# Performance work log

Hardware: AMD Instinct MI355X
Metric: run time of the kernel (lower is better)

Reference implementation:

```python
import jax, jax.numpy as jnp
import numpy as np

B, D, NCOMP, DCOMP = 4096, 2048, 4, 1024  # out_features = NCOMP * DCOMP = 4096


def setup_inputs() -> dict:
    key = jax.random.key(0)
    ks = jax.random.split(key, 6)
    scale = 0.02
    return {
        "x": jax.random.normal(ks[0], (B, D), jnp.float32),
        "noise": jax.random.normal(ks[1], (B, NCOMP), jnp.float32),
        "Wc": jax.random.normal(ks[2], (NCOMP, D, DCOMP), jnp.float32) * scale,
        "bc": jnp.zeros((NCOMP, DCOMP), jnp.float32),
        "Wg": jax.random.normal(ks[3], (D, NCOMP), jnp.float32) * scale,
        "bg": jnp.zeros((NCOMP,), jnp.float32),
        "Wn": jax.random.normal(ks[4], (D, NCOMP), jnp.float32) * scale,
        "bn": jnp.zeros((NCOMP,), jnp.float32),
    }


def reference(x, noise, Wc, bc, Wg, bg, Wn, bn):
    # gating: H = Wg(x) + randn * softplus(Wnoise(x))
    g = x @ Wg + bg                                   # [B, n]
    sp = jax.nn.softplus(x @ Wn + bn)                 # [B, n]
    H = g + noise * sp                                # [B, n]
    # top-1 index, monotonic hard gate: select all components i <= argmax
    k = jnp.argmax(H, axis=1, keepdims=True)          # [B, 1]
    mask = (jnp.arange(H.shape[1])[None, :] <= k).astype(H.dtype)  # [B, n]
    # straight-through: forward value = mask, grad d G/d H = identity
    G = H + jax.lax.stop_gradient(mask - H)
    # all components computed vectorized; unselected ones are zeroed by G
    comps = jnp.einsum('bd,ndo->bno', x, Wc) + bc     # [B, n, DCOMP]
    mask_sg = jax.lax.stop_gradient(mask)
    # multiply by mask_sg so unselected (padded) channels carry no grad path,
    # matching torch which never computes components beyond k (zero pad).
    E = (comps * G[:, :, None] * mask_sg[:, :, None]).reshape(x.shape[0], -1)  # [B, out_features]
    return (E, G)
```

## Files before the change

kernel.cpp:

```cpp
#include <hip/hip_runtime.h>
#include <hip/hip_bf16.h>
#include <math.h>

constexpr int BROWS = 4096;
constexpr int DDIM  = 2048;
constexpr int NCOMP = 4;
constexpr int DCOMP = 1024;
constexpr int NOUT  = NCOMP * DCOMP;

typedef __attribute__((ext_vector_type(8))) short bf16x8;
typedef __attribute__((ext_vector_type(4))) float f32x4;
typedef __attribute__((ext_vector_type(4))) short s16x4;

__device__ __forceinline__ short f2bf(float f) {
  union { float f; unsigned u; } v; v.f = f;
  unsigned r = v.u + 0x7FFFu + ((v.u >> 16) & 1u);
  return (short)(r >> 16);
}

#define GLOAD_LDS16(gptr, lptr) __builtin_amdgcn_global_load_lds( \
    (const __attribute__((address_space(1))) void*)(gptr),        \
    (__attribute__((address_space(3))) void*)(lptr), 16, 0, 0)

__global__ __launch_bounds__(256) void prep_kernel(
    const float* __restrict__ x, const float* __restrict__ noise,
    const float* __restrict__ Wg, const float* __restrict__ bg,
    const float* __restrict__ Wn, const float* __restrict__ bn,
    const float* __restrict__ Wc,
    float* __restrict__ Gout, short* __restrict__ xb, short* __restrict__ WcT) {
  __shared__ float tile[64][65];
  const int bid = blockIdx.x;
  const int tid = threadIdx.x;

  if (bid < 1024) {
    const int lane = tid & 63;
    const int row  = bid * 4 + (tid >> 6);
    const float* xr = x + (size_t)row * DDIM;
    short* xbr = xb + (size_t)row * DDIM;

    float ag[4] = {0.f, 0.f, 0.f, 0.f};
    float an[4] = {0.f, 0.f, 0.f, 0.f};
#pragma unroll
    for (int i = 0; i < 8; i++) {
      int d = i * 256 + lane * 4;
      float4 v = *reinterpret_cast<const float4*>(xr + d);
      s16x4 s; s.x = f2bf(v.x); s.y = f2bf(v.y); s.z = f2bf(v.z); s.w = f2bf(v.w);
      *reinterpret_cast<s16x4*>(xbr + d) = s;
      float xv[4] = {v.x, v.y, v.z, v.w};
#pragma unroll
      for (int j = 0; j < 4; j++) {
        float4 wg = *reinterpret_cast<const float4*>(Wg + 4 * (d + j));
        float4 wn = *reinterpret_cast<const float4*>(Wn + 4 * (d + j));
        ag[0] += xv[j] * wg.x; ag[1] += xv[j] * wg.y;
        ag[2] += xv[j] * wg.z; ag[3] += xv[j] * wg.w;
        an[0] += xv[j] * wn.x; an[1] += xv[j] * wn.y;
        an[2] += xv[j] * wn.z; an[3] += xv[j] * wn.w;
      }
    }
#pragma unroll
    for (int off = 32; off > 0; off >>= 1) {
#pragma unroll
      for (int c = 0; c < 4; c++) {
        ag[c] += __shfl_xor(ag[c], off);
        an[c] += __shfl_xor(an[c], off);
      }
    }
    if (lane == 0) {
      float H[4];
#pragma unroll
      for (int c = 0; c < 4; c++) {
        float v  = an[c] + bn[c];
        float sp = (v > 20.f) ? v : log1pf(expf(v));
        H[c] = (ag[c] + bg[c]) + noise[(size_t)row * NCOMP + c] * sp;
      }
      int k = 0; float best = H[0];
#pragma unroll
      for (int c = 1; c < 4; c++) { if (H[c] > best) { best = H[c]; k = c; } }
#pragma unroll
      for (int c = 0; c < 4; c++)
        Gout[(size_t)row * NCOMP + c] = (c <= k) ? 1.0f : 0.0f;
    }
  } else {
    const int tb  = bid - 1024;
    const int o_t = tb & 15, d_t = (tb >> 4) & 31, c = tb >> 9;
    const int d0 = d_t * 64, o0 = o_t * 64;
    const int col = tid & 63, rb = tid >> 6;

    const float* src = Wc + ((size_t)c * DDIM + d0) * DCOMP + o0;
#pragma unroll
    for (int i = 0; i < 16; i++) {
      int r = rb + i * 4;
      tile[r][col] = src[(size_t)r * DCOMP + col];
    }
    __syncthreads();
    short* dst = WcT + ((size_t)c * DCOMP + o0) * DDIM + d0;
    const int o   = tid >> 2;
    const int dsb = (tid & 3) * 16;
    bf16x8 p0, p1;
#pragma unroll
    for (int k = 0; k < 8; k++) {
      p0[k] = f2bf(tile[dsb + k][o]);
      p1[k] = f2bf(tile[dsb + 8 + k][o]);
    }
    *reinterpret_cast<bf16x8*>(dst + (size_t)o * DDIM + dsb)     = p0;
    *reinterpret_cast<bf16x8*>(dst + (size_t)o * DDIM + dsb + 8) = p1;
  }
}

constexpr int BM = 256, BN = 256, BK = 64;
constexpr int NT = DDIM / BK;
constexpr int HS = 128 * 64;

template<int MB, int NB>
__device__ __forceinline__ void MF(f32x4 (&acc)[8][4], bf16x8 (&a)[4][2], bf16x8 (&b)[2][2]) {
#pragma unroll
  for (int kh = 0; kh < 2; kh++)
#pragma unroll
    for (int ml = 0; ml < 4; ml++)
#pragma unroll
      for (int nl = 0; nl < 2; nl++)
        acc[MB + ml][NB + nl] = __builtin_amdgcn_mfma_f32_16x16x32_bf16(
            a[ml][kh], b[nl][kh], acc[MB + ml][NB + nl], 0, 0, 0);
}

#define PH_SYNC_MFMA(MB, NB, BREG)                           \
  __builtin_amdgcn_sched_barrier(0);                         \
  __builtin_amdgcn_s_barrier();                              \
  asm volatile("s_waitcnt lgkmcnt(0)");                      \
  __builtin_amdgcn_s_setprio(1);                             \
  MF<MB, NB>(acc, a, BREG);                                  \
  __builtin_amdgcn_s_setprio(0);

__global__ __launch_bounds__(512, 2) void gemm_kernel(
    const short* __restrict__ xb, const short* __restrict__ wt,
    const float* __restrict__ bc, const float* __restrict__ G,
    float* __restrict__ E) {
  __shared__ short Asm[2][2][HS];
  __shared__ short Bsm[2][2][HS];

  const int tid  = threadIdx.x;
  const int wave = tid >> 6, lane = tid & 63;
  const int wm = wave >> 2, wn = wave & 3;
  const int fr = lane & 15, fq = lane >> 4, l7 = lane & 7;

  const int xcd = blockIdx.x & 7, j = blockIdx.x >> 3;
  const int trow0 = (((xcd >> 1) << 2) + (j & 3)) * BM;
  const int tcol0 = (((xcd & 1) << 3) + (j >> 2)) * BN;

  const short* baseA[2] = { xb + (size_t)(trow0      ) * DDIM,
                            xb + (size_t)(trow0 + 128) * DDIM };
  const short* baseB[2] = { wt + (size_t)(tcol0      ) * DDIM,
                            wt + (size_t)(tcol0 + 128) * DDIM };

  size_t soff[2]; int ldst[2];
#pragma unroll
  for (int l = 0; l < 2; l++) {
    int f = l * 512 + tid;
    int r = f >> 3;
    int s = (f & 7) ^ (r & 7);
    soff[l] = (size_t)r * DDIM + s * 8;
    ldst[l] = (l * 512 + wave * 64) * 8;
  }

  auto STAGE = [&](const short* gb, int t, short* ldsh) {
#pragma unroll
    for (int l = 0; l < 2; l++)
      GLOAD_LDS16(gb + t * 64 + soff[l], ldsh + ldst[l]);
  };
  auto LDA = [&](const short* Ah, bf16x8 (&a)[4][2]) {
#pragma unroll
    for (int ml = 0; ml < 4; ml++) {
      int rh = wm * 64 + ml * 16 + fr;
#pragma unroll
      for (int kh = 0; kh < 2; kh++) {
        int sl = ((kh * 4 + fq) ^ l7) * 8;
        a[ml][kh] = *reinterpret_cast<const bf16x8*>(Ah + rh * 64 + sl);
      }
    }
  };
  auto LDB = [&](const short* Bh, bf16x8 (&b)[2][2]) {
#pragma unroll
    for (int nl = 0; nl < 2; nl++) {
      int ch = wn * 32 + nl * 16 + fr;
#pragma unroll
      for (int kh = 0; kh < 2; kh++) {
        int sl = ((kh * 4 + fq) ^ l7) * 8;
        b[nl][kh] = *reinterpret_cast<const bf16x8*>(Bh + ch * 64 + sl);
      }
    }
  };

  f32x4 acc[8][4];
#pragma unroll
  for (int m = 0; m < 8; m++)
#pragma unroll
    for (int n = 0; n < 4; n++) acc[m][n] = f32x4{0.f, 0.f, 0.f, 0.f};
  bf16x8 a[4][2], bA[2][2], bB[2][2];

  STAGE(baseA[0], 0, &Asm[0][0][0]);
  STAGE(baseB[0], 0, &Bsm[0][0][0]);
  STAGE(baseB[1], 0, &Bsm[0][1][0]);
  STAGE(baseA[1], 0, &Asm[0][1][0]);
  STAGE(baseA[0], 1, &Asm[1][0][0]);
  STAGE(baseB[0], 1, &Bsm[1][0][0]);
  STAGE(baseB[1], 1, &Bsm[1][1][0]);
  asm volatile("s_waitcnt vmcnt(6)" ::: "memory");
  __builtin_amdgcn_s_barrier();

  for (int i = 0; i < NT / 2 - 1; i++) {
    const int t1 = 2 * i + 1, t2 = 2 * i + 2, t3 = 2 * i + 3;

    LDA(&Asm[0][0][0], a); LDB(&Bsm[0][0][0], bA);
    STAGE(baseA[1], t1, &Asm[1][1][0]);
    PH_SYNC_MFMA(0, 0, bA);
    __builtin_amdgcn_s_barrier();
    LDB(&Bsm[0][1][0], bB);
    STAGE(baseA[0], t2, &Asm[0][0][0]);
    PH_SYNC_MFMA(0, 2, bB);
    __builtin_amdgcn_s_barrier();
    LDA(&Asm[0][1][0], a);
    STAGE(baseB[0], t2, &Bsm[0][0][0]);
    PH_SYNC_MFMA(4, 2, bB);
    __builtin_amdgcn_s_barrier();
    STAGE(baseB[1], t2, &Bsm[0][1][0]);
    PH_SYNC_MFMA(4, 0, bA);
    asm volatile("s_waitcnt vmcnt(6)" ::: "memory");
    __builtin_amdgcn_s_barrier();
    LDA(&Asm[1][0][0], a); LDB(&Bsm[1][0][0], bA);
    STAGE(baseA[1], t2, &Asm[0][1][0]);
    PH_SYNC_MFMA(0, 0, bA);
    __builtin_amdgcn_s_barrier();
    LDB(&Bsm[1][1][0], bB);
    STAGE(baseA[0], t3, &Asm[1][0][0]);
    PH_SYNC_MFMA(0, 2, bB);
    __builtin_amdgcn_s_barrier();
    LDA(&Asm[1][1][0], a);
    STAGE(baseB[0], t3, &Bsm[1][0][0]);
    PH_SYNC_MFMA(4, 2, bB);
    __builtin_amdgcn_s_barrier();
    STAGE(baseB[1], t3, &Bsm[1][1][0]);
    PH_SYNC_MFMA(4, 0, bA);
    asm volatile("s_waitcnt vmcnt(6)" ::: "memory");
    __builtin_amdgcn_s_barrier();
  }

  {
    LDA(&Asm[0][0][0], a); LDB(&Bsm[0][0][0], bA);
    STAGE(baseA[1], NT - 1, &Asm[1][1][0]);
    PH_SYNC_MFMA(0, 0, bA);
    __builtin_amdgcn_s_barrier();
    LDB(&Bsm[0][1][0], bB);
    PH_SYNC_MFMA(0, 2, bB);
    __builtin_amdgcn_s_barrier();
    LDA(&Asm[0][1][0], a);
    PH_SYNC_MFMA(4, 2, bB);
    __builtin_amdgcn_s_barrier();
    PH_SYNC_MFMA(4, 0, bA);
    asm volatile("s_waitcnt vmcnt(0)" ::: "memory");
    __builtin_amdgcn_s_barrier();
    LDA(&Asm[1][0][0], a); LDB(&Bsm[1][0][0], bA);
    PH_SYNC_MFMA(0, 0, bA);
    __builtin_amdgcn_s_barrier();
    LDB(&Bsm[1][1][0], bB);
    PH_SYNC_MFMA(0, 2, bB);
    __builtin_amdgcn_s_barrier();
    LDA(&Asm[1][1][0], a);
    PH_SYNC_MFMA(4, 2, bB);
    __builtin_amdgcn_s_barrier();
    PH_SYNC_MFMA(4, 0, bA);
  }

  const int comp = tcol0 >> 10;
  const float* __restrict__ bcn = bc + (size_t)comp * DCOMP + (tcol0 & (DCOMP - 1));
  float bias[4];
#pragma unroll
  for (int n = 0; n < 4; n++)
    bias[n] = bcn[((n >> 1) * 128) + wn * 32 + (n & 1) * 16 + fr];
#pragma unroll
  for (int m = 0; m < 8; m++) {
    int growb = trow0 + ((m >> 2) * 128) + wm * 64 + (m & 3) * 16 + fq * 4;
#pragma unroll
    for (int j2 = 0; j2 < 4; j2++) {
      int r = growb + j2;
      float mval = G[(size_t)r * NCOMP + comp];
      float* Erow = E + (size_t)r * NOUT + tcol0;
#pragma unroll
      for (int n = 0; n < 4; n++) {
        int coll = ((n >> 1) * 128) + wn * 32 + (n & 1) * 16 + fr;
        Erow[coll] = mval * (acc[m][n][j2] + bias[n]);
      }
    }
  }
}

extern "C" void kernel_launch(void* const* d_in, const int* in_sizes, int n_in,
                              void* d_out, int out_size, void* d_ws, size_t ws_size,
                              hipStream_t stream) {
  const float* x     = (const float*)d_in[0];
  const float* noise = (const float*)d_in[1];
  const float* Wc    = (const float*)d_in[2];
  const float* bc    = (const float*)d_in[3];
  const float* Wg    = (const float*)d_in[4];
  const float* bg    = (const float*)d_in[5];
  const float* Wn    = (const float*)d_in[6];
  const float* bn    = (const float*)d_in[7];

  float* E = (float*)d_out;
  float* G = (float*)d_out + (size_t)BROWS * NOUT;

  short* xb  = (short*)d_ws;
  short* WcT = xb + (size_t)BROWS * DDIM;

  prep_kernel<<<3072, 256, 0, stream>>>(x, noise, Wg, bg, Wn, bn, Wc, G, xb, WcT);
  gemm_kernel<<<256, 512, 0, stream>>>(xb, WcT, bc, G, E);
}
```

Measured before the change: 91.72 us.

## Merge last two MFMA phases per tile and loosen LDS waits in GEMM pipeline

Fuses the third and fourth MFMA phases of each K-tile into one phase, so each tile has fewer workgroup barriers, and issues both B-tile stages together beforehand. Removes the sched_barrier before each phase and adds a partial lgkmcnt wait before the first phase of each tile. The aim is to cut barrier and scheduling overhead in the main loop. In exchange, the compiler gets more freedom to reorder, and the two merged stages put more load traffic into one window, which could upset the overlap between LDS reads and global loads.

```diff
diff --git a/kernel.cpp b/kernel.cpp
--- a/kernel.cpp
+++ b/kernel.cpp
@@ -111,8 +111,10 @@
 constexpr int NT = DDIM / BK;
 constexpr int HS = 128 * 64;
 
+#define BAR __builtin_amdgcn_s_barrier()
+
 template<int MB, int NB>
-__device__ __forceinline__ void MF(f32x4 (&acc)[8][4], bf16x8 (&a)[4][2], bf16x8 (&b)[2][2]) {
+__device__ __forceinline__ void MFc(f32x4 (&acc)[8][4], bf16x8 (&a)[4][2], bf16x8 (&b)[2][2]) {
 #pragma unroll
   for (int kh = 0; kh < 2; kh++)
 #pragma unroll
@@ -123,12 +125,19 @@
             a[ml][kh], b[nl][kh], acc[MB + ml][NB + nl], 0, 0, 0);
 }
 
-#define PH_SYNC_MFMA(MB, NB, BREG)                           \
-  __builtin_amdgcn_sched_barrier(0);                         \
-  __builtin_amdgcn_s_barrier();                              \
+#define PH16(MB, NB, BREG)                                   \
+  BAR;                                                       \
   asm volatile("s_waitcnt lgkmcnt(0)");                      \
   __builtin_amdgcn_s_setprio(1);                             \
-  MF<MB, NB>(acc, a, BREG);                                  \
+  MFc<MB, NB>(acc, a, BREG);                                 \
+  __builtin_amdgcn_s_setprio(0);
+
+#define PH32(BREG1, BREG0)                                   \
+  BAR;                                                       \
+  asm volatile("s_waitcnt lgkmcnt(0)");                      \
+  __builtin_amdgcn_s_setprio(1);                             \
+  MFc<4, 2>(acc, a, BREG1);                                  \
+  MFc<4, 0>(acc, a, BREG0);                                  \
   __builtin_amdgcn_s_setprio(0);
 
 __global__ __launch_bounds__(512, 2) void gemm_kernel(
@@ -205,69 +214,63 @@
   STAGE(baseB[0], 1, &Bsm[1][0][0]);
   STAGE(baseB[1], 1, &Bsm[1][1][0]);
   asm volatile("s_waitcnt vmcnt(6)" ::: "memory");
-  __builtin_amdgcn_s_barrier();
+  BAR;
 
   for (int i = 0; i < NT / 2 - 1; i++) {
     const int t1 = 2 * i + 1, t2 = 2 * i + 2, t3 = 2 * i + 3;
 
     LDA(&Asm[0][0][0], a); LDB(&Bsm[0][0][0], bA);
     STAGE(baseA[1], t1, &Asm[1][1][0]);
-    PH_SYNC_MFMA(0, 0, bA);
-    __builtin_amdgcn_s_barrier();
+    asm volatile("s_waitcnt lgkmcnt(8)");
+    PH16(0, 0, bA);
+    BAR;
     LDB(&Bsm[0][1][0], bB);
     STAGE(baseA[0], t2, &Asm[0][0][0]);
-    PH_SYNC_MFMA(0, 2, bB);
-    __builtin_amdgcn_s_barrier();
+    PH16(0, 2, bB);
+    BAR;
     LDA(&Asm[0][1][0], a);
-    STAGE(baseB[0], t2, &Bsm[0][0][0]);
-    PH_SYNC_MFMA(4, 2, bB);
-    __builtin_amdgcn_s_barrier();
-    STAGE(baseB[1], t2, &Bsm[0][1][0]);
-    PH_SYNC_MFMA(4, 0, bA);
+    STAGE(baseB[0], t2, &Bsm[0][0][0]); STAGE(baseB[1], t2, &Bsm[0][1][0]);
+    PH32(bB, bA);
     asm volatile("s_waitcnt vmcnt(6)" ::: "memory");
-    __builtin_amdgcn_s_barrier();
+    BAR;
     LDA(&Asm[1][0][0], a); LDB(&Bsm[1][0][0], bA);
     STAGE(baseA[1], t2, &Asm[0][1][0]);
-    PH_SYNC_MFMA(0, 0, bA);
-    __builtin_amdgcn_s_barrier();
+    asm volatile("s_waitcnt lgkmcnt(8)");
+    PH16(0, 0, bA);
+    BAR;
     LDB(&Bsm[1][1][0], bB);
     STAGE(baseA[0], t3, &Asm[1][0][0]);
-    PH_SYNC_MFMA(0, 2, bB);
-    __builtin_amdgcn_s_barrier();
+    PH16(0, 2, bB);
+    BAR;
     LDA(&Asm[1][1][0], a);
-    STAGE(baseB[0], t3, &Bsm[1][0][0]);
-    PH_SYNC_MFMA(4, 2, bB);
-    __builtin_amdgcn_s_barrier();
-    STAGE(baseB[1], t3, &Bsm[1][1][0]);
-    PH_SYNC_MFMA(4, 0, bA);
+    STAGE(baseB[0], t3, &Bsm[1][0][0]); STAGE(baseB[1], t3, &Bsm[1][1][0]);
+    PH32(bB, bA);
     asm volatile("s_waitcnt vmcnt(6)" ::: "memory");
-    __builtin_amdgcn_s_barrier();
+    BAR;
   }
 
   {
     LDA(&Asm[0][0][0], a); LDB(&Bsm[0][0][0], bA);
     STAGE(baseA[1], NT - 1, &Asm[1][1][0]);
-    PH_SYNC_MFMA(0, 0, bA);
-    __builtin_amdgcn_s_barrier();
+    asm volatile("s_waitcnt lgkmcnt(8)");
+    PH16(0, 0, bA);
+    BAR;
     LDB(&Bsm[0][1][0], bB);
-    PH_SYNC_MFMA(0, 2, bB);
-    __builtin_amdgcn_s_barrier();
+    PH16(0, 2, bB);
+    BAR;
     LDA(&Asm[0][1][0], a);
-    PH_SYNC_MFMA(4, 2, bB);
-    __builtin_amdgcn_s_barrier();
-    PH_SYNC_MFMA(4, 0, bA);
+    PH32(bB, bA);
     asm volatile("s_waitcnt vmcnt(0)" ::: "memory");
-    __builtin_amdgcn_s_barrier();
+    BAR;
     LDA(&Asm[1][0][0], a); LDB(&Bsm[1][0][0], bA);
-    PH_SYNC_MFMA(0, 0, bA);
-    __builtin_amdgcn_s_barrier();
+    asm volatile("s_waitcnt lgkmcnt(8)");
+    PH16(0, 0, bA);
+    BAR;
     LDB(&Bsm[1][1][0], bB);
-    PH_SYNC_MFMA(0, 2, bB);
-    __builtin_amdgcn_s_barrier();
+    PH16(0, 2, bB);
+    BAR;
     LDA(&Asm[1][1][0], a);
-    PH_SYNC_MFMA(4, 2, bB);
-    __builtin_amdgcn_s_barrier();
-    PH_SYNC_MFMA(4, 0, bA);
+    PH32(bB, bA);
   }
 
   const int comp = tcol0 >> 10;
```

After: 91.78 us. About the same (+0.1%).
